# Kernel optimization log

Hardware: AMD Instinct MI355X
Metric: run time of the kernel (lower is better)

The kernel has to match this reference:

```python
import jax, jax.numpy as jnp
import numpy as np

B, NNODES = 65536, 32
D_IN, D_G, D_C, H, D_OUT = 16, 8, 16, 64, 4


def setup_inputs() -> dict:
    key = jax.random.key(0)
    ks = jax.random.split(key, 24)
    N = B * NNODES
    x = jax.random.normal(ks[0], (N, D_IN), jnp.float32)
    other_obs = jax.random.normal(ks[1], (B, D_C), jnp.float32)
    # star graph per batch element with reverse edges: (0->j) and (j->0)
    bs = np.concatenate([np.zeros(NNODES - 1, np.int32), np.arange(1, NNODES, dtype=np.int32)])
    bd = np.concatenate([np.arange(1, NNODES, dtype=np.int32), np.zeros(NNODES - 1, np.int32)])
    offs = (np.arange(B, dtype=np.int32) * NNODES)[:, None]
    src = jnp.asarray((bs[None, :] + offs).reshape(-1))
    dst = jnp.asarray((bd[None, :] + offs).reshape(-1))
    node_seg = jnp.asarray(np.repeat(np.arange(B, dtype=np.int32), NNODES))
    s = 0.1
    p = lambda k, sh: jax.random.normal(k, sh, jnp.float32) * s
    return dict(
        x=x, other_obs=other_obs, src=src, dst=dst, node_seg=node_seg,
        Wp1=p(ks[2], (D_IN, D_G)), bp1=jnp.zeros((D_G,), jnp.float32),
        Ws1=p(ks[3], (D_IN, D_G)), Wn1=p(ks[4], (D_G, D_G)), bc1=jnp.zeros((D_G,), jnp.float32),
        Wp2=p(ks[5], (D_G, D_G)), bp2=jnp.zeros((D_G,), jnp.float32),
        Ws2=p(ks[6], (D_G, D_G)), Wn2=p(ks[7], (D_G, D_G)), bc2=jnp.zeros((D_G,), jnp.float32),
        W1=p(ks[8], (D_C + D_G, H)), bf1=jnp.zeros((H,), jnp.float32),
        W2=p(ks[9], (H, H)), bf2=jnp.zeros((H,), jnp.float32),
        W3=p(ks[10], (H, H)), bf3=jnp.zeros((H,), jnp.float32),
        W4=jax.random.uniform(ks[11], (H, D_OUT), jnp.float32, -0.003, 0.003),
        bf4=jnp.zeros((D_OUT,), jnp.float32),
    )


def _sage_pool(h, src, dst, Wp, bp, Ws, Wn, bc, num_nodes):
    # DGL SAGEConv aggregator_type='pool': relu(fc_pool(h_src)), scatter-max to dst
    m = jax.nn.relu(h @ Wp + bp)[src]              # [E, D_G]
    agg = jax.ops.segment_max(m, dst, num_segments=num_nodes)
    agg = jnp.where(jnp.isfinite(agg), agg, 0.0)   # empty-neighbor nodes -> 0 (DGL default)
    return h @ Ws + agg @ Wn + bc


def reference(x, other_obs, src, dst, node_seg,
              Wp1, bp1, Ws1, Wn1, bc1,
              Wp2, bp2, Ws2, Wn2, bc2,
              W1, bf1, W2, bf2, W3, bf3, W4, bf4):
    N = x.shape[0]
    Bn = other_obs.shape[0]
    n_per = N // Bn
    h = jnp.tanh(_sage_pool(x, src, dst, Wp1, bp1, Ws1, Wn1, bc1, N))  # conv1 activation=tanh
    h = _sage_pool(h, src, dst, Wp2, bp2, Ws2, Wn2, bc2, N)            # conv2, no activation
    pooled = jax.ops.segment_sum(h, node_seg, num_segments=Bn) / n_per  # AvgPooling (fixed n)
    res = jnp.concatenate([pooled, other_obs], axis=1)
    h1 = jax.nn.relu(res @ W1 + bf1)
    h2 = jax.nn.relu(h1 @ W2 + bf2)
    h3 = jax.nn.relu(h2 @ W3 + bf3)
    return jnp.tanh(h3 @ W4 + bf4)
```

## Files before the change

### kernel.cpp

```cpp
#include <hip/hip_runtime.h>


typedef float v2f __attribute__((ext_vector_type(2)));
__device__ __forceinline__ v2f fma2(v2f a, v2f b, v2f c) {
  return __builtin_elementwise_fma(a, b, c);
}
__device__ __forceinline__ v2f ld2(const float* p) { return *(const v2f*)p; }

__device__ __forceinline__ float fast_tanh(float v) {
  v = fminf(fmaxf(v, -10.f), 10.f);
  float e = exp2f(v * 2.8853900817779268f);
  return 1.f - 2.f * __builtin_amdgcn_rcpf(e + 1.f);
}

template<int CTRL, int RMASK>
__device__ __forceinline__ float dpp0(float v) {
  return __int_as_float(__builtin_amdgcn_update_dpp(
      0, __float_as_int(v), CTRL, RMASK, 0xf, true));
}
__device__ __forceinline__ float red_max32(float t) {
  t = fmaxf(t, dpp0<0x111, 0xf>(t));
  t = fmaxf(t, dpp0<0x112, 0xf>(t));
  t = fmaxf(t, dpp0<0x114, 0xf>(t));
  t = fmaxf(t, dpp0<0x118, 0xf>(t));
  t = fmaxf(t, dpp0<0x142, 0xa>(t));
  return t;
}
__device__ __forceinline__ float red_sum32(float t) {
  t += dpp0<0x111, 0xf>(t);
  t += dpp0<0x112, 0xf>(t);
  t += dpp0<0x114, 0xf>(t);
  t += dpp0<0x118, 0xf>(t);
  t += dpp0<0x142, 0xa>(t);
  return t;
}
__device__ __forceinline__ float bcast31(float v) {
  return __int_as_float(__builtin_amdgcn_ds_swizzle(__float_as_int(v), 0x03E0));
}

__global__ __launch_bounds__(256, 4) void conv_kernel(
    const float* __restrict__ x,
    const float* __restrict__ Wp1, const float* __restrict__ bp1,
    const float* __restrict__ Ws1, const float* __restrict__ Wn1,
    const float* __restrict__ bc1,
    const float* __restrict__ Wp2, const float* __restrict__ bp2,
    float* __restrict__ res) {
  const int lane = threadIdx.x & 63;
  const int pair = blockIdx.x * 4 + (threadIdx.x >> 6);
  const int nl = lane & 31, s = lane >> 5;
  const int node = 31 - nl;
  const int b = pair * 2 + s;
  const bool isn0 = (nl == 31);

  const float4* xp = (const float4*)(x + ((size_t)b * 32 + node) * 16);
  float4 a0 = xp[0], a1 = xp[1], a2 = xp[2], a3 = xp[3];
  float xr[16] = {a0.x,a0.y,a0.z,a0.w, a1.x,a1.y,a1.z,a1.w,
                  a2.x,a2.y,a2.z,a2.w, a3.x,a3.y,a3.z,a3.w};

  v2f mv[4], sv[4];
  #pragma unroll
  for (int i = 0; i < 4; i++) { mv[i] = ld2(bp1 + 2*i); sv[i] = ld2(bc1 + 2*i); }
  #pragma unroll
  for (int f = 0; f < 16; f++) {
    v2f xv = {xr[f], xr[f]};
    #pragma unroll
    for (int i = 0; i < 4; i++) {
      mv[i] = fma2(xv, ld2(Wp1 + f*8 + 2*i), mv[i]);
      sv[i] = fma2(xv, ld2(Ws1 + f*8 + 2*i), sv[i]);
    }
  }
  float m[8];
  #pragma unroll
  for (int i = 0; i < 4; i++) {
    m[2*i]   = fmaxf(mv[i].x, 0.f);
    m[2*i+1] = fmaxf(mv[i].y, 0.f);
  }

  float agg[8];
  #pragma unroll
  for (int g = 0; g < 8; g++) {
    float t = isn0 ? 0.f : m[g];
    t = red_max32(t);
    float b0v = bcast31(m[g]);
    agg[g] = isn0 ? t : b0v;
  }
  #pragma unroll
  for (int j = 0; j < 8; j++) {
    v2f av = {agg[j], agg[j]};
    #pragma unroll
    for (int i = 0; i < 4; i++) sv[i] = fma2(av, ld2(Wn1 + j*8 + 2*i), sv[i]);
  }
  float h[8];
  #pragma unroll
  for (int i = 0; i < 4; i++) {
    h[2*i]   = fast_tanh(sv[i].x);
    h[2*i+1] = fast_tanh(sv[i].y);
  }

  v2f m2v[4];
  #pragma unroll
  for (int i = 0; i < 4; i++) m2v[i] = ld2(bp2 + 2*i);
  #pragma unroll
  for (int j = 0; j < 8; j++) {
    v2f hv = {h[j], h[j]};
    #pragma unroll
    for (int i = 0; i < 4; i++) m2v[i] = fma2(hv, ld2(Wp2 + j*8 + 2*i), m2v[i]);
  }
  float m2[8];
  #pragma unroll
  for (int i = 0; i < 4; i++) {
    m2[2*i]   = fmaxf(m2v[i].x, 0.f);
    m2[2*i+1] = fmaxf(m2v[i].y, 0.f);
  }

  float outv[16];
  #pragma unroll
  for (int g = 0; g < 8; g++) outv[g] = red_sum32(h[g]);
  #pragma unroll
  for (int g = 0; g < 8; g++) {
    float t = isn0 ? 0.f : m2[g];
    t = red_max32(t);
    outv[8+g] = fmaf(31.f, m2[g], t);
  }
  if (isn0) {
    float4* rp = (float4*)(res + (size_t)b * 16);
    rp[0] = make_float4(outv[0],  outv[1],  outv[2],  outv[3]);
    rp[1] = make_float4(outv[4],  outv[5],  outv[6],  outv[7]);
    rp[2] = make_float4(outv[8],  outv[9],  outv[10], outv[11]);
    rp[3] = make_float4(outv[12], outv[13], outv[14], outv[15]);
  }
}

#define HSTR 65
__global__ __launch_bounds__(256, 3) void mlp_kernel(
    const float* __restrict__ res, const float* __restrict__ obs,
    const float* __restrict__ Ws2, const float* __restrict__ Wn2,
    const float* __restrict__ bc2,
    const float* __restrict__ W1, const float* __restrict__ bf1,
    const float* __restrict__ W2, const float* __restrict__ bf2,
    const float* __restrict__ W3, const float* __restrict__ bf3,
    const float* __restrict__ W4, const float* __restrict__ bf4,
    float* __restrict__ out) {
  __shared__ float hx[64 * HSTR];
  const int tid  = threadIdx.x;
  const int lane = tid & 63;
  const int p    = __builtin_amdgcn_readfirstlane(tid >> 6);
  const int b    = blockIdx.x * 64 + lane;
  const int ob0  = p * 16;

  const float4* rp = (const float4*)(res + (size_t)b * 16);
  float4 r0 = rp[0], r1 = rp[1], r2 = rp[2], r3 = rp[3];
  const float4* op = (const float4*)(obs + (size_t)b * 16);
  float4 o0 = op[0], o1 = op[1], o2 = op[2], o3 = op[3];
  float rm[8] = {r0.x,r0.y,r0.z,r0.w, r1.x,r1.y,r1.z,r1.w};
  float ag[8] = {r2.x,r2.y,r2.z,r2.w, r3.x,r3.y,r3.z,r3.w};
  float ob[16] = {o0.x,o0.y,o0.z,o0.w, o1.x,o1.y,o1.z,o1.w,
                  o2.x,o2.y,o2.z,o2.w, o3.x,o3.y,o3.z,o3.w};

  v2f pv[4];
  #pragma unroll
  for (int i = 0; i < 4; i++) pv[i] = (v2f){0.f, 0.f};
  #pragma unroll
  for (int j = 0; j < 8; j++) {
    v2f rv = {rm[j], rm[j]}, av = {ag[j], ag[j]};
    #pragma unroll
    for (int i = 0; i < 4; i++) {
      pv[i] = fma2(rv, ld2(Ws2 + j*8 + 2*i), pv[i]);
      pv[i] = fma2(av, ld2(Wn2 + j*8 + 2*i), pv[i]);
    }
  }
  float pooled[8];
  #pragma unroll
  for (int i = 0; i < 4; i++) {
    pooled[2*i]   = fmaf(pv[i].x, 1.f/32.f, bc2[2*i]);
    pooled[2*i+1] = fmaf(pv[i].y, 1.f/32.f, bc2[2*i+1]);
  }

  v2f acc[8];
  #pragma unroll
  for (int i = 0; i < 8; i++) acc[i] = ld2(bf1 + ob0 + 2*i);
  #pragma unroll
  for (int j = 0; j < 8; j++) {
    v2f sj = {pooled[j], pooled[j]};
    #pragma unroll
    for (int i = 0; i < 8; i++) acc[i] = fma2(sj, ld2(W1 + j*64 + ob0 + 2*i), acc[i]);
  }
  #pragma unroll
  for (int j = 0; j < 16; j++) {
    v2f sj = {ob[j], ob[j]};
    #pragma unroll
    for (int i = 0; i < 8; i++) acc[i] = fma2(sj, ld2(W1 + (8+j)*64 + ob0 + 2*i), acc[i]);
  }
  #pragma unroll
  for (int i = 0; i < 8; i++) {
    hx[lane*HSTR + ob0 + 2*i]   = fmaxf(acc[i].x, 0.f);
    hx[lane*HSTR + ob0 + 2*i+1] = fmaxf(acc[i].y, 0.f);
  }
  __syncthreads();
  float h[64];
  #pragma unroll
  for (int k = 0; k < 64; k++) h[k] = hx[lane*HSTR + k];
  __syncthreads();

  #pragma unroll
  for (int i = 0; i < 8; i++) acc[i] = ld2(bf2 + ob0 + 2*i);
  #pragma unroll
  for (int k = 0; k < 64; k++) {
    v2f hk = {h[k], h[k]};
    #pragma unroll
    for (int i = 0; i < 8; i++) acc[i] = fma2(hk, ld2(W2 + k*64 + ob0 + 2*i), acc[i]);
  }
  #pragma unroll
  for (int i = 0; i < 8; i++) {
    hx[lane*HSTR + ob0 + 2*i]   = fmaxf(acc[i].x, 0.f);
    hx[lane*HSTR + ob0 + 2*i+1] = fmaxf(acc[i].y, 0.f);
  }
  __syncthreads();
  #pragma unroll
  for (int k = 0; k < 64; k++) h[k] = hx[lane*HSTR + k];
  __syncthreads();

  #pragma unroll
  for (int i = 0; i < 8; i++) acc[i] = ld2(bf3 + ob0 + 2*i);
  #pragma unroll
  for (int k = 0; k < 64; k++) {
    v2f hk = {h[k], h[k]};
    #pragma unroll
    for (int i = 0; i < 8; i++) acc[i] = fma2(hk, ld2(W3 + k*64 + ob0 + 2*i), acc[i]);
  }
  #pragma unroll
  for (int i = 0; i < 8; i++) {
    hx[lane*HSTR + ob0 + 2*i]   = fmaxf(acc[i].x, 0.f);
    hx[lane*HSTR + ob0 + 2*i+1] = fmaxf(acc[i].y, 0.f);
  }
  __syncthreads();

  if (p == 0) {
    #pragma unroll
    for (int k = 0; k < 64; k++) h[k] = hx[lane*HSTR + k];
    v2f o4a = ld2(bf4), o4b = ld2(bf4 + 2);
    #pragma unroll
    for (int k = 0; k < 64; k++) {
      v2f hk = {h[k], h[k]};
      o4a = fma2(hk, ld2(W4 + k*4),     o4a);
      o4b = fma2(hk, ld2(W4 + k*4 + 2), o4b);
    }
    ((float4*)out)[b] = make_float4(fast_tanh(o4a.x), fast_tanh(o4a.y),
                                    fast_tanh(o4b.x), fast_tanh(o4b.y));
  }
}

extern "C" void kernel_launch(void* const* d_in, const int* in_sizes, int n_in,
                              void* d_out, int out_size, void* d_ws, size_t ws_size,
                              hipStream_t stream) {
  const float* x   = (const float*)d_in[0];
  const float* obs = (const float*)d_in[1];
  const float* Wp1 = (const float*)d_in[5];
  const float* bp1 = (const float*)d_in[6];
  const float* Ws1 = (const float*)d_in[7];
  const float* Wn1 = (const float*)d_in[8];
  const float* bc1 = (const float*)d_in[9];
  const float* Wp2 = (const float*)d_in[10];
  const float* bp2 = (const float*)d_in[11];
  const float* Ws2 = (const float*)d_in[12];
  const float* Wn2 = (const float*)d_in[13];
  const float* bc2 = (const float*)d_in[14];
  const float* W1  = (const float*)d_in[15];
  const float* bf1 = (const float*)d_in[16];
  const float* W2  = (const float*)d_in[17];
  const float* bf2 = (const float*)d_in[18];
  const float* W3  = (const float*)d_in[19];
  const float* bf3 = (const float*)d_in[20];
  const float* W4  = (const float*)d_in[21];
  const float* bf4 = (const float*)d_in[22];
  float* res = (float*)d_ws;
  float* out = (float*)d_out;

  hipLaunchKernelGGL(conv_kernel, dim3(8192), dim3(256), 0, stream,
                     x, Wp1, bp1, Ws1, Wn1, bc1, Wp2, bp2, res);
  hipLaunchKernelGGL(mlp_kernel, dim3(1024), dim3(256), 0, stream,
                     res, obs, Ws2, Wn2, bc2, W1, bf1, W2, bf2, W3, bf3, W4, bf4, out);
}
```

Baseline: 280.0 us.

## Fuse conv and MLP kernels into one kernel with shared-memory handoff

Merges the graph-conv kernel and the MLP kernel into a single launch. Each 256-thread block now loops over 8 batch pairs per wave, prefetching the next x tile while it computes the current one, and stages the per-graph results in shared memory instead of a global workspace. This removes one launch and the global write and read of the intermediate. In exchange the grid drops to 1024 blocks with serialized conv work per wave, the launch bound rises from 3 to 4 blocks per CU for the MLP part, and register and LDS pressure both increase.

After: 299.6 us. 1.07x slower.

```diff
diff --git a/kernel.cpp b/kernel.cpp
--- a/kernel.cpp
+++ b/kernel.cpp
@@ -38,122 +38,130 @@
   return __int_as_float(__builtin_amdgcn_ds_swizzle(__float_as_int(v), 0x03E0));
 }
 
-__global__ __launch_bounds__(256, 4) void conv_kernel(
-    const float* __restrict__ x,
+#define RSTR 17
+#define HSTR 65
+
+__global__ __launch_bounds__(256, 4) void fused_gnn(
+    const float* __restrict__ x,   const float* __restrict__ obs,
     const float* __restrict__ Wp1, const float* __restrict__ bp1,
     const float* __restrict__ Ws1, const float* __restrict__ Wn1,
     const float* __restrict__ bc1,
     const float* __restrict__ Wp2, const float* __restrict__ bp2,
-    float* __restrict__ res) {
-  const int lane = threadIdx.x & 63;
-  const int pair = blockIdx.x * 4 + (threadIdx.x >> 6);
-  const int nl = lane & 31, s = lane >> 5;
-  const int node = 31 - nl;
-  const int b = pair * 2 + s;
-  const bool isn0 = (nl == 31);
-
-  const float4* xp = (const float4*)(x + ((size_t)b * 32 + node) * 16);
-  float4 a0 = xp[0], a1 = xp[1], a2 = xp[2], a3 = xp[3];
-  float xr[16] = {a0.x,a0.y,a0.z,a0.w, a1.x,a1.y,a1.z,a1.w,
-                  a2.x,a2.y,a2.z,a2.w, a3.x,a3.y,a3.z,a3.w};
-
-  v2f mv[4], sv[4];
-  #pragma unroll
-  for (int i = 0; i < 4; i++) { mv[i] = ld2(bp1 + 2*i); sv[i] = ld2(bc1 + 2*i); }
-  #pragma unroll
-  for (int f = 0; f < 16; f++) {
-    v2f xv = {xr[f], xr[f]};
-    #pragma unroll
-    for (int i = 0; i < 4; i++) {
-      mv[i] = fma2(xv, ld2(Wp1 + f*8 + 2*i), mv[i]);
-      sv[i] = fma2(xv, ld2(Ws1 + f*8 + 2*i), sv[i]);
-    }
-  }
-  float m[8];
-  #pragma unroll
-  for (int i = 0; i < 4; i++) {
-    m[2*i]   = fmaxf(mv[i].x, 0.f);
-    m[2*i+1] = fmaxf(mv[i].y, 0.f);
-  }
-
-  float agg[8];
-  #pragma unroll
-  for (int g = 0; g < 8; g++) {
-    float t = isn0 ? 0.f : m[g];
-    t = red_max32(t);
-    float b0v = bcast31(m[g]);
-    agg[g] = isn0 ? t : b0v;
-  }
-  #pragma unroll
-  for (int j = 0; j < 8; j++) {
-    v2f av = {agg[j], agg[j]};
-    #pragma unroll
-    for (int i = 0; i < 4; i++) sv[i] = fma2(av, ld2(Wn1 + j*8 + 2*i), sv[i]);
-  }
-  float h[8];
-  #pragma unroll
-  for (int i = 0; i < 4; i++) {
-    h[2*i]   = fast_tanh(sv[i].x);
-    h[2*i+1] = fast_tanh(sv[i].y);
-  }
-
-  v2f m2v[4];
-  #pragma unroll
-  for (int i = 0; i < 4; i++) m2v[i] = ld2(bp2 + 2*i);
-  #pragma unroll
-  for (int j = 0; j < 8; j++) {
-    v2f hv = {h[j], h[j]};
-    #pragma unroll
-    for (int i = 0; i < 4; i++) m2v[i] = fma2(hv, ld2(Wp2 + j*8 + 2*i), m2v[i]);
-  }
-  float m2[8];
-  #pragma unroll
-  for (int i = 0; i < 4; i++) {
-    m2[2*i]   = fmaxf(m2v[i].x, 0.f);
-    m2[2*i+1] = fmaxf(m2v[i].y, 0.f);
-  }
-
-  float outv[16];
-  #pragma unroll
-  for (int g = 0; g < 8; g++) outv[g] = red_sum32(h[g]);
-  #pragma unroll
-  for (int g = 0; g < 8; g++) {
-    float t = isn0 ? 0.f : m2[g];
-    t = red_max32(t);
-    outv[8+g] = fmaf(31.f, m2[g], t);
-  }
-  if (isn0) {
-    float4* rp = (float4*)(res + (size_t)b * 16);
-    rp[0] = make_float4(outv[0],  outv[1],  outv[2],  outv[3]);
-    rp[1] = make_float4(outv[4],  outv[5],  outv[6],  outv[7]);
-    rp[2] = make_float4(outv[8],  outv[9],  outv[10], outv[11]);
-    rp[3] = make_float4(outv[12], outv[13], outv[14], outv[15]);
-  }
-}
-
-#define HSTR 65
-__global__ __launch_bounds__(256, 3) void mlp_kernel(
-    const float* __restrict__ res, const float* __restrict__ obs,
     const float* __restrict__ Ws2, const float* __restrict__ Wn2,
     const float* __restrict__ bc2,
-    const float* __restrict__ W1, const float* __restrict__ bf1,
-    const float* __restrict__ W2, const float* __restrict__ bf2,
-    const float* __restrict__ W3, const float* __restrict__ bf3,
-    const float* __restrict__ W4, const float* __restrict__ bf4,
+    const float* __restrict__ W1,  const float* __restrict__ bf1,
+    const float* __restrict__ W2,  const float* __restrict__ bf2,
+    const float* __restrict__ W3,  const float* __restrict__ bf3,
+    const float* __restrict__ W4,  const float* __restrict__ bf4,
     float* __restrict__ out) {
+  __shared__ float resT[64 * RSTR];
   __shared__ float hx[64 * HSTR];
+
   const int tid  = threadIdx.x;
   const int lane = tid & 63;
   const int p    = __builtin_amdgcn_readfirstlane(tid >> 6);
-  const int b    = blockIdx.x * 64 + lane;
-  const int ob0  = p * 16;
-
-  const float4* rp = (const float4*)(res + (size_t)b * 16);
-  float4 r0 = rp[0], r1 = rp[1], r2 = rp[2], r3 = rp[3];
-  const float4* op = (const float4*)(obs + (size_t)b * 16);
+  const int nl   = lane & 31, s = lane >> 5;
+  const int node = 31 - nl;
+  const bool isn0 = (nl == 31);
+  const int b0   = blockIdx.x * 64;
+
+  const float4* op = (const float4*)(obs + (size_t)(b0 + lane) * 16);
   float4 o0 = op[0], o1 = op[1], o2 = op[2], o3 = op[3];
-  float rm[8] = {r0.x,r0.y,r0.z,r0.w, r1.x,r1.y,r1.z,r1.w};
-  float ag[8] = {r2.x,r2.y,r2.z,r2.w, r3.x,r3.y,r3.z,r3.w};
+
+  const float* xb = x + (((size_t)(b0 + p * 16 + s)) * 32 + node) * 16;
+  float4 c0, c1, c2, c3;
+  { const float4* xp = (const float4*)xb; c0 = xp[0]; c1 = xp[1]; c2 = xp[2]; c3 = xp[3]; }
+
+  for (int j = 0; j < 8; ++j) {
+    float4 nx0, nx1, nx2, nx3;
+    if (j < 7) {
+      const float4* xp = (const float4*)(xb + (size_t)(j + 1) * 1024);
+      nx0 = xp[0]; nx1 = xp[1]; nx2 = xp[2]; nx3 = xp[3];
+    }
+    float xr[16] = {c0.x,c0.y,c0.z,c0.w, c1.x,c1.y,c1.z,c1.w,
+                    c2.x,c2.y,c2.z,c2.w, c3.x,c3.y,c3.z,c3.w};
+
+    v2f mv[4], sv[4];
+    #pragma unroll
+    for (int i = 0; i < 4; i++) { mv[i] = ld2(bp1 + 2*i); sv[i] = ld2(bc1 + 2*i); }
+    #pragma unroll
+    for (int f = 0; f < 16; f++) {
+      v2f xv = {xr[f], xr[f]};
+      #pragma unroll
+      for (int i = 0; i < 4; i++) {
+        mv[i] = fma2(xv, ld2(Wp1 + f*8 + 2*i), mv[i]);
+        sv[i] = fma2(xv, ld2(Ws1 + f*8 + 2*i), sv[i]);
+      }
+    }
+    float m[8];
+    #pragma unroll
+    for (int i = 0; i < 4; i++) {
+      m[2*i]   = fmaxf(mv[i].x, 0.f);
+      m[2*i+1] = fmaxf(mv[i].y, 0.f);
+    }
+
+    float agg[8];
+    #pragma unroll
+    for (int g = 0; g < 8; g++) {
+      float t = isn0 ? 0.f : m[g];
+      t = red_max32(t);
+      float b0v = bcast31(m[g]);
+      agg[g] = isn0 ? t : b0v;
+    }
+    #pragma unroll
+    for (int jj = 0; jj < 8; jj++) {
+      v2f av = {agg[jj], agg[jj]};
+      #pragma unroll
+      for (int i = 0; i < 4; i++) sv[i] = fma2(av, ld2(Wn1 + jj*8 + 2*i), sv[i]);
+    }
+    float h[8];
+    #pragma unroll
+    for (int i = 0; i < 4; i++) {
+      h[2*i]   = fast_tanh(sv[i].x);
+      h[2*i+1] = fast_tanh(sv[i].y);
+    }
+
+    v2f m2v[4];
+    #pragma unroll
+    for (int i = 0; i < 4; i++) m2v[i] = ld2(bp2 + 2*i);
+    #pragma unroll
+    for (int jj = 0; jj < 8; jj++) {
+      v2f hv = {h[jj], h[jj]};
+      #pragma unroll
+      for (int i = 0; i < 4; i++) m2v[i] = fma2(hv, ld2(Wp2 + jj*8 + 2*i), m2v[i]);
+    }
+    float m2[8];
+    #pragma unroll
+    for (int i = 0; i < 4; i++) {
+      m2[2*i]   = fmaxf(m2v[i].x, 0.f);
+      m2[2*i+1] = fmaxf(m2v[i].y, 0.f);
+    }
+
+    float outv[16];
+    #pragma unroll
+    for (int g = 0; g < 8; g++) outv[g] = red_sum32(h[g]);
+    #pragma unroll
+    for (int g = 0; g < 8; g++) {
+      float t = isn0 ? 0.f : m2[g];
+      t = red_max32(t);
+      outv[8+g] = fmaf(31.f, m2[g], t);
+    }
+    if (isn0) {
+      const int bib = (p * 8 + j) * 2 + s;
+      #pragma unroll
+      for (int i = 0; i < 16; i++) resT[bib * RSTR + i] = outv[i];
+    }
+    if (j < 7) { c0 = nx0; c1 = nx1; c2 = nx2; c3 = nx3; }
+  }
+  __syncthreads();
+
+  const int ob0 = p * 16;
+  float rm[8], ag[8];
+  #pragma unroll
+  for (int jj = 0; jj < 8; jj++) {
+    rm[jj] = resT[lane * RSTR + jj];
+    ag[jj] = resT[lane * RSTR + 8 + jj];
+  }
   float ob[16] = {o0.x,o0.y,o0.z,o0.w, o1.x,o1.y,o1.z,o1.w,
                   o2.x,o2.y,o2.z,o2.w, o3.x,o3.y,o3.z,o3.w};
 
@@ -161,12 +169,12 @@
   #pragma unroll
   for (int i = 0; i < 4; i++) pv[i] = (v2f){0.f, 0.f};
   #pragma unroll
-  for (int j = 0; j < 8; j++) {
-    v2f rv = {rm[j], rm[j]}, av = {ag[j], ag[j]};
-    #pragma unroll
-    for (int i = 0; i < 4; i++) {
-      pv[i] = fma2(rv, ld2(Ws2 + j*8 + 2*i), pv[i]);
-      pv[i] = fma2(av, ld2(Wn2 + j*8 + 2*i), pv[i]);
+  for (int jj = 0; jj < 8; jj++) {
+    v2f rv = {rm[jj], rm[jj]}, av = {ag[jj], ag[jj]};
+    #pragma unroll
+    for (int i = 0; i < 4; i++) {
+      pv[i] = fma2(rv, ld2(Ws2 + jj*8 + 2*i), pv[i]);
+      pv[i] = fma2(av, ld2(Wn2 + jj*8 + 2*i), pv[i]);
     }
   }
   float pooled[8];
@@ -180,16 +188,16 @@
   #pragma unroll
   for (int i = 0; i < 8; i++) acc[i] = ld2(bf1 + ob0 + 2*i);
   #pragma unroll
-  for (int j = 0; j < 8; j++) {
-    v2f sj = {pooled[j], pooled[j]};
-    #pragma unroll
-    for (int i = 0; i < 8; i++) acc[i] = fma2(sj, ld2(W1 + j*64 + ob0 + 2*i), acc[i]);
-  }
-  #pragma unroll
-  for (int j = 0; j < 16; j++) {
-    v2f sj = {ob[j], ob[j]};
-    #pragma unroll
-    for (int i = 0; i < 8; i++) acc[i] = fma2(sj, ld2(W1 + (8+j)*64 + ob0 + 2*i), acc[i]);
+  for (int jj = 0; jj < 8; jj++) {
+    v2f sj = {pooled[jj], pooled[jj]};
+    #pragma unroll
+    for (int i = 0; i < 8; i++) acc[i] = fma2(sj, ld2(W1 + jj*64 + ob0 + 2*i), acc[i]);
+  }
+  #pragma unroll
+  for (int jj = 0; jj < 16; jj++) {
+    v2f sj = {ob[jj], ob[jj]};
+    #pragma unroll
+    for (int i = 0; i < 8; i++) acc[i] = fma2(sj, ld2(W1 + (8+jj)*64 + ob0 + 2*i), acc[i]);
   }
   #pragma unroll
   for (int i = 0; i < 8; i++) {
@@ -245,8 +253,8 @@
       o4a = fma2(hk, ld2(W4 + k*4),     o4a);
       o4b = fma2(hk, ld2(W4 + k*4 + 2), o4b);
     }
-    ((float4*)out)[b] = make_float4(fast_tanh(o4a.x), fast_tanh(o4a.y),
-                                    fast_tanh(o4b.x), fast_tanh(o4b.y));
+    ((float4*)out)[b0 + lane] = make_float4(fast_tanh(o4a.x), fast_tanh(o4a.y),
+                                            fast_tanh(o4b.x), fast_tanh(o4b.y));
   }
 }
 
@@ -273,11 +281,9 @@
   const float* bf3 = (const float*)d_in[20];
   const float* W4  = (const float*)d_in[21];
   const float* bf4 = (const float*)d_in[22];
-  float* res = (float*)d_ws;
   float* out = (float*)d_out;
 
-  hipLaunchKernelGGL(conv_kernel, dim3(8192), dim3(256), 0, stream,
-                     x, Wp1, bp1, Ws1, Wn1, bc1, Wp2, bp2, res);
-  hipLaunchKernelGGL(mlp_kernel, dim3(1024), dim3(256), 0, stream,
-                     res, obs, Ws2, Wn2, bc2, W1, bf1, W2, bf2, W3, bf3, W4, bf4, out);
-}
+  hipLaunchKernelGGL(fused_gnn, dim3(1024), dim3(256), 0, stream,
+                     x, obs, Wp1, bp1, Ws1, Wn1, bc1, Wp2, bp2, Ws2, Wn2, bc2,
+                     W1, bf1, W2, bf2, W3, bf3, W4, bf4, out);
+}
```

## Process two graph pairs per wave in conv and split MLP across eight waves

Applied to the files above, without the earlier changes.

The conv kernel now has each wave handle two pairs of batch elements. All x loads for both are issued up front so memory latency overlaps across the unrolled iterations, and the grid is halved. The MLP kernel moves to 512-thread blocks where each wave computes 8 output columns instead of 16, which cuts per-thread accumulator registers and adds more waves per block. The tanh input clamp is also removed; it relied on rcp handling large exponents, and the unclamped exp2 can overflow to inf for large inputs.

After: 293.8 us. 4.9% more time.

```diff
diff --git a/kernel.cpp b/kernel.cpp
--- a/kernel.cpp
+++ b/kernel.cpp
@@ -8,7 +8,6 @@
 __device__ __forceinline__ v2f ld2(const float* p) { return *(const v2f*)p; }
 
 __device__ __forceinline__ float fast_tanh(float v) {
-  v = fminf(fmaxf(v, -10.f), 10.f);
   float e = exp2f(v * 2.8853900817779268f);
   return 1.f - 2.f * __builtin_amdgcn_rcpf(e + 1.f);
 }
@@ -46,93 +45,105 @@
     const float* __restrict__ Wp2, const float* __restrict__ bp2,
     float* __restrict__ res) {
   const int lane = threadIdx.x & 63;
-  const int pair = blockIdx.x * 4 + (threadIdx.x >> 6);
+  const int wid  = blockIdx.x * 4 + (threadIdx.x >> 6);
   const int nl = lane & 31, s = lane >> 5;
   const int node = 31 - nl;
-  const int b = pair * 2 + s;
   const bool isn0 = (nl == 31);
 
-  const float4* xp = (const float4*)(x + ((size_t)b * 32 + node) * 16);
-  float4 a0 = xp[0], a1 = xp[1], a2 = xp[2], a3 = xp[3];
-  float xr[16] = {a0.x,a0.y,a0.z,a0.w, a1.x,a1.y,a1.z,a1.w,
-                  a2.x,a2.y,a2.z,a2.w, a3.x,a3.y,a3.z,a3.w};
-
-  v2f mv[4], sv[4];
-  #pragma unroll
-  for (int i = 0; i < 4; i++) { mv[i] = ld2(bp1 + 2*i); sv[i] = ld2(bc1 + 2*i); }
-  #pragma unroll
-  for (int f = 0; f < 16; f++) {
-    v2f xv = {xr[f], xr[f]};
-    #pragma unroll
-    for (int i = 0; i < 4; i++) {
-      mv[i] = fma2(xv, ld2(Wp1 + f*8 + 2*i), mv[i]);
-      sv[i] = fma2(xv, ld2(Ws1 + f*8 + 2*i), sv[i]);
-    }
-  }
-  float m[8];
-  #pragma unroll
-  for (int i = 0; i < 4; i++) {
-    m[2*i]   = fmaxf(mv[i].x, 0.f);
-    m[2*i+1] = fmaxf(mv[i].y, 0.f);
-  }
-
-  float agg[8];
-  #pragma unroll
-  for (int g = 0; g < 8; g++) {
-    float t = isn0 ? 0.f : m[g];
-    t = red_max32(t);
-    float b0v = bcast31(m[g]);
-    agg[g] = isn0 ? t : b0v;
-  }
-  #pragma unroll
-  for (int j = 0; j < 8; j++) {
-    v2f av = {agg[j], agg[j]};
-    #pragma unroll
-    for (int i = 0; i < 4; i++) sv[i] = fma2(av, ld2(Wn1 + j*8 + 2*i), sv[i]);
-  }
-  float h[8];
-  #pragma unroll
-  for (int i = 0; i < 4; i++) {
-    h[2*i]   = fast_tanh(sv[i].x);
-    h[2*i+1] = fast_tanh(sv[i].y);
-  }
-
-  v2f m2v[4];
-  #pragma unroll
-  for (int i = 0; i < 4; i++) m2v[i] = ld2(bp2 + 2*i);
-  #pragma unroll
-  for (int j = 0; j < 8; j++) {
-    v2f hv = {h[j], h[j]};
-    #pragma unroll
-    for (int i = 0; i < 4; i++) m2v[i] = fma2(hv, ld2(Wp2 + j*8 + 2*i), m2v[i]);
-  }
-  float m2[8];
-  #pragma unroll
-  for (int i = 0; i < 4; i++) {
-    m2[2*i]   = fmaxf(m2v[i].x, 0.f);
-    m2[2*i+1] = fmaxf(m2v[i].y, 0.f);
-  }
-
-  float outv[16];
-  #pragma unroll
-  for (int g = 0; g < 8; g++) outv[g] = red_sum32(h[g]);
-  #pragma unroll
-  for (int g = 0; g < 8; g++) {
-    float t = isn0 ? 0.f : m2[g];
-    t = red_max32(t);
-    outv[8+g] = fmaf(31.f, m2[g], t);
-  }
-  if (isn0) {
-    float4* rp = (float4*)(res + (size_t)b * 16);
-    rp[0] = make_float4(outv[0],  outv[1],  outv[2],  outv[3]);
-    rp[1] = make_float4(outv[4],  outv[5],  outv[6],  outv[7]);
-    rp[2] = make_float4(outv[8],  outv[9],  outv[10], outv[11]);
-    rp[3] = make_float4(outv[12], outv[13], outv[14], outv[15]);
+  const int bA = wid * 4 + s;
+  const float* xbA = x + (((size_t)bA) * 32 + node) * 16;
+  const float* xbB = xbA + 2 * 32 * 16;
+
+  const float4* xpA = (const float4*)xbA;
+  const float4* xpB = (const float4*)xbB;
+  float4 A0 = xpA[0], A1 = xpA[1], A2 = xpA[2], A3 = xpA[3];
+  float4 B0 = xpB[0], B1 = xpB[1], B2 = xpB[2], B3 = xpB[3];
+
+  #pragma unroll
+  for (int pp = 0; pp < 2; ++pp) {
+    const int b = (pp == 0) ? bA : bA + 2;
+    float4 c0 = (pp == 0) ? A0 : B0, c1 = (pp == 0) ? A1 : B1;
+    float4 c2 = (pp == 0) ? A2 : B2, c3 = (pp == 0) ? A3 : B3;
+    float xr[16] = {c0.x,c0.y,c0.z,c0.w, c1.x,c1.y,c1.z,c1.w,
+                    c2.x,c2.y,c2.z,c2.w, c3.x,c3.y,c3.z,c3.w};
+
+    v2f mv[4], sv[4];
+    #pragma unroll
+    for (int i = 0; i < 4; i++) { mv[i] = ld2(bp1 + 2*i); sv[i] = ld2(bc1 + 2*i); }
+    #pragma unroll
+    for (int f = 0; f < 16; f++) {
+      v2f xv = {xr[f], xr[f]};
+      #pragma unroll
+      for (int i = 0; i < 4; i++) {
+        mv[i] = fma2(xv, ld2(Wp1 + f*8 + 2*i), mv[i]);
+        sv[i] = fma2(xv, ld2(Ws1 + f*8 + 2*i), sv[i]);
+      }
+    }
+    float m[8];
+    #pragma unroll
+    for (int i = 0; i < 4; i++) {
+      m[2*i]   = fmaxf(mv[i].x, 0.f);
+      m[2*i+1] = fmaxf(mv[i].y, 0.f);
+    }
+
+    float agg[8];
+    #pragma unroll
+    for (int g = 0; g < 8; g++) {
+      float t = isn0 ? 0.f : m[g];
+      t = red_max32(t);
+      float b0v = bcast31(m[g]);
+      agg[g] = isn0 ? t : b0v;
+    }
+    #pragma unroll
+    for (int jj = 0; jj < 8; jj++) {
+      v2f av = {agg[jj], agg[jj]};
+      #pragma unroll
+      for (int i = 0; i < 4; i++) sv[i] = fma2(av, ld2(Wn1 + jj*8 + 2*i), sv[i]);
+    }
+    float h[8];
+    #pragma unroll
+    for (int i = 0; i < 4; i++) {
+      h[2*i]   = fast_tanh(sv[i].x);
+      h[2*i+1] = fast_tanh(sv[i].y);
+    }
+
+    v2f m2v[4];
+    #pragma unroll
+    for (int i = 0; i < 4; i++) m2v[i] = ld2(bp2 + 2*i);
+    #pragma unroll
+    for (int jj = 0; jj < 8; jj++) {
+      v2f hv = {h[jj], h[jj]};
+      #pragma unroll
+      for (int i = 0; i < 4; i++) m2v[i] = fma2(hv, ld2(Wp2 + jj*8 + 2*i), m2v[i]);
+    }
+    float m2[8];
+    #pragma unroll
+    for (int i = 0; i < 4; i++) {
+      m2[2*i]   = fmaxf(m2v[i].x, 0.f);
+      m2[2*i+1] = fmaxf(m2v[i].y, 0.f);
+    }
+
+    float outv[16];
+    #pragma unroll
+    for (int g = 0; g < 8; g++) outv[g] = red_sum32(h[g]);
+    #pragma unroll
+    for (int g = 0; g < 8; g++) {
+      float t = isn0 ? 0.f : m2[g];
+      t = red_max32(t);
+      outv[8+g] = fmaf(31.f, m2[g], t);
+    }
+    if (isn0) {
+      float4* rp = (float4*)(res + (size_t)b * 16);
+      rp[0] = make_float4(outv[0],  outv[1],  outv[2],  outv[3]);
+      rp[1] = make_float4(outv[4],  outv[5],  outv[6],  outv[7]);
+      rp[2] = make_float4(outv[8],  outv[9],  outv[10], outv[11]);
+      rp[3] = make_float4(outv[12], outv[13], outv[14], outv[15]);
+    }
   }
 }
 
 #define HSTR 65
-__global__ __launch_bounds__(256, 3) void mlp_kernel(
+__global__ __launch_bounds__(512, 2) void mlp_kernel(
     const float* __restrict__ res, const float* __restrict__ obs,
     const float* __restrict__ Ws2, const float* __restrict__ Wn2,
     const float* __restrict__ bc2,
@@ -146,7 +157,7 @@
   const int lane = tid & 63;
   const int p    = __builtin_amdgcn_readfirstlane(tid >> 6);
   const int b    = blockIdx.x * 64 + lane;
-  const int ob0  = p * 16;
+  const int ob0  = p * 8;
 
   const float4* rp = (const float4*)(res + (size_t)b * 16);
   float4 r0 = rp[0], r1 = rp[1], r2 = rp[2], r3 = rp[3];
@@ -161,12 +172,12 @@
   #pragma unroll
   for (int i = 0; i < 4; i++) pv[i] = (v2f){0.f, 0.f};
   #pragma unroll
-  for (int j = 0; j < 8; j++) {
-    v2f rv = {rm[j], rm[j]}, av = {ag[j], ag[j]};
-    #pragma unroll
-    for (int i = 0; i < 4; i++) {
-      pv[i] = fma2(rv, ld2(Ws2 + j*8 + 2*i), pv[i]);
-      pv[i] = fma2(av, ld2(Wn2 + j*8 + 2*i), pv[i]);
+  for (int jj = 0; jj < 8; jj++) {
+    v2f rv = {rm[jj], rm[jj]}, av = {ag[jj], ag[jj]};
+    #pragma unroll
+    for (int i = 0; i < 4; i++) {
+      pv[i] = fma2(rv, ld2(Ws2 + jj*8 + 2*i), pv[i]);
+      pv[i] = fma2(av, ld2(Wn2 + jj*8 + 2*i), pv[i]);
     }
   }
   float pooled[8];
@@ -176,23 +187,23 @@
     pooled[2*i+1] = fmaf(pv[i].y, 1.f/32.f, bc2[2*i+1]);
   }
 
-  v2f acc[8];
-  #pragma unroll
-  for (int i = 0; i < 8; i++) acc[i] = ld2(bf1 + ob0 + 2*i);
-  #pragma unroll
-  for (int j = 0; j < 8; j++) {
-    v2f sj = {pooled[j], pooled[j]};
-    #pragma unroll
-    for (int i = 0; i < 8; i++) acc[i] = fma2(sj, ld2(W1 + j*64 + ob0 + 2*i), acc[i]);
-  }
-  #pragma unroll
-  for (int j = 0; j < 16; j++) {
-    v2f sj = {ob[j], ob[j]};
-    #pragma unroll
-    for (int i = 0; i < 8; i++) acc[i] = fma2(sj, ld2(W1 + (8+j)*64 + ob0 + 2*i), acc[i]);
-  }
-  #pragma unroll
-  for (int i = 0; i < 8; i++) {
+  v2f acc[4];
+  #pragma unroll
+  for (int i = 0; i < 4; i++) acc[i] = ld2(bf1 + ob0 + 2*i);
+  #pragma unroll
+  for (int jj = 0; jj < 8; jj++) {
+    v2f sj = {pooled[jj], pooled[jj]};
+    #pragma unroll
+    for (int i = 0; i < 4; i++) acc[i] = fma2(sj, ld2(W1 + jj*64 + ob0 + 2*i), acc[i]);
+  }
+  #pragma unroll
+  for (int jj = 0; jj < 16; jj++) {
+    v2f sj = {ob[jj], ob[jj]};
+    #pragma unroll
+    for (int i = 0; i < 4; i++) acc[i] = fma2(sj, ld2(W1 + (8+jj)*64 + ob0 + 2*i), acc[i]);
+  }
+  #pragma unroll
+  for (int i = 0; i < 4; i++) {
     hx[lane*HSTR + ob0 + 2*i]   = fmaxf(acc[i].x, 0.f);
     hx[lane*HSTR + ob0 + 2*i+1] = fmaxf(acc[i].y, 0.f);
   }
@@ -203,15 +214,15 @@
   __syncthreads();
 
   #pragma unroll
-  for (int i = 0; i < 8; i++) acc[i] = ld2(bf2 + ob0 + 2*i);
+  for (int i = 0; i < 4; i++) acc[i] = ld2(bf2 + ob0 + 2*i);
   #pragma unroll
   for (int k = 0; k < 64; k++) {
     v2f hk = {h[k], h[k]};
     #pragma unroll
-    for (int i = 0; i < 8; i++) acc[i] = fma2(hk, ld2(W2 + k*64 + ob0 + 2*i), acc[i]);
-  }
-  #pragma unroll
-  for (int i = 0; i < 8; i++) {
+    for (int i = 0; i < 4; i++) acc[i] = fma2(hk, ld2(W2 + k*64 + ob0 + 2*i), acc[i]);
+  }
+  #pragma unroll
+  for (int i = 0; i < 4; i++) {
     hx[lane*HSTR + ob0 + 2*i]   = fmaxf(acc[i].x, 0.f);
     hx[lane*HSTR + ob0 + 2*i+1] = fmaxf(acc[i].y, 0.f);
   }
@@ -221,15 +232,15 @@
   __syncthreads();
 
   #pragma unroll
-  for (int i = 0; i < 8; i++) acc[i] = ld2(bf3 + ob0 + 2*i);
+  for (int i = 0; i < 4; i++) acc[i] = ld2(bf3 + ob0 + 2*i);
   #pragma unroll
   for (int k = 0; k < 64; k++) {
     v2f hk = {h[k], h[k]};
     #pragma unroll
-    for (int i = 0; i < 8; i++) acc[i] = fma2(hk, ld2(W3 + k*64 + ob0 + 2*i), acc[i]);
-  }
-  #pragma unroll
-  for (int i = 0; i < 8; i++) {
+    for (int i = 0; i < 4; i++) acc[i] = fma2(hk, ld2(W3 + k*64 + ob0 + 2*i), acc[i]);
+  }
+  #pragma unroll
+  for (int i = 0; i < 4; i++) {
     hx[lane*HSTR + ob0 + 2*i]   = fmaxf(acc[i].x, 0.f);
     hx[lane*HSTR + ob0 + 2*i+1] = fmaxf(acc[i].y, 0.f);
   }
@@ -276,8 +287,8 @@
   float* res = (float*)d_ws;
   float* out = (float*)d_out;
 
-  hipLaunchKernelGGL(conv_kernel, dim3(8192), dim3(256), 0, stream,
+  hipLaunchKernelGGL(conv_kernel, dim3(4096), dim3(256), 0, stream,
                      x, Wp1, bp1, Ws1, Wn1, bc1, Wp2, bp2, res);
-  hipLaunchKernelGGL(mlp_kernel, dim3(1024), dim3(256), 0, stream,
+  hipLaunchKernelGGL(mlp_kernel, dim3(1024), dim3(512), 0, stream,
                      res, obs, Ws2, Wn2, bc2, W1, bf1, W2, bf2, W3, bf3, W4, bf4, out);
 }
```

## Process two batch rows per thread in MLP kernel to reuse weight loads

Applied to the files above, without the earlier changes.

The MLP kernel now handles 128 batch rows per block, so each thread computes two rows and every weight load feeds two sets of accumulators. The first stage (pooled plus obs) is computed by half the threads and staged in shared memory, and activations are read from LDS inside the loops instead of being copied into a register array. The grid is halved to match. The tanh input clamp is also dropped to save instructions, which relies on exp2f overflow still giving the right saturated values, and shared memory and register use go up, which may lower occupancy.

Measured after the change: 282.1 us. No clear change (+0.7%).

```diff
diff --git a/kernel.cpp b/kernel.cpp
--- a/kernel.cpp
+++ b/kernel.cpp
@@ -8,7 +8,6 @@
 __device__ __forceinline__ v2f ld2(const float* p) { return *(const v2f*)p; }
 
 __device__ __forceinline__ float fast_tanh(float v) {
-  v = fminf(fmaxf(v, -10.f), 10.f);
   float e = exp2f(v * 2.8853900817779268f);
   return 1.f - 2.f * __builtin_amdgcn_rcpf(e + 1.f);
 }
@@ -49,8 +48,8 @@
   const int pair = blockIdx.x * 4 + (threadIdx.x >> 6);
   const int nl = lane & 31, s = lane >> 5;
   const int node = 31 - nl;
+  const bool isn0 = (nl == 31);
   const int b = pair * 2 + s;
-  const bool isn0 = (nl == 31);
 
   const float4* xp = (const float4*)(x + ((size_t)b * 32 + node) * 16);
   float4 a0 = xp[0], a1 = xp[1], a2 = xp[2], a3 = xp[3];
@@ -85,10 +84,10 @@
     agg[g] = isn0 ? t : b0v;
   }
   #pragma unroll
-  for (int j = 0; j < 8; j++) {
-    v2f av = {agg[j], agg[j]};
-    #pragma unroll
-    for (int i = 0; i < 4; i++) sv[i] = fma2(av, ld2(Wn1 + j*8 + 2*i), sv[i]);
+  for (int jj = 0; jj < 8; jj++) {
+    v2f av = {agg[jj], agg[jj]};
+    #pragma unroll
+    for (int i = 0; i < 4; i++) sv[i] = fma2(av, ld2(Wn1 + jj*8 + 2*i), sv[i]);
   }
   float h[8];
   #pragma unroll
@@ -101,10 +100,10 @@
   #pragma unroll
   for (int i = 0; i < 4; i++) m2v[i] = ld2(bp2 + 2*i);
   #pragma unroll
-  for (int j = 0; j < 8; j++) {
-    v2f hv = {h[j], h[j]};
-    #pragma unroll
-    for (int i = 0; i < 4; i++) m2v[i] = fma2(hv, ld2(Wp2 + j*8 + 2*i), m2v[i]);
+  for (int jj = 0; jj < 8; jj++) {
+    v2f hv = {h[jj], h[jj]};
+    #pragma unroll
+    for (int i = 0; i < 4; i++) m2v[i] = fma2(hv, ld2(Wp2 + jj*8 + 2*i), m2v[i]);
   }
   float m2[8];
   #pragma unroll
@@ -131,7 +130,8 @@
   }
 }
 
-#define HSTR 65
+#define H0S 25
+#define HXS 65
 __global__ __launch_bounds__(256, 3) void mlp_kernel(
     const float* __restrict__ res, const float* __restrict__ obs,
     const float* __restrict__ Ws2, const float* __restrict__ Wn2,
@@ -141,112 +141,133 @@
     const float* __restrict__ W3, const float* __restrict__ bf3,
     const float* __restrict__ W4, const float* __restrict__ bf4,
     float* __restrict__ out) {
-  __shared__ float hx[64 * HSTR];
+  __shared__ float h0[128 * H0S];
+  __shared__ float hx[128 * HXS];
   const int tid  = threadIdx.x;
   const int lane = tid & 63;
   const int p    = __builtin_amdgcn_readfirstlane(tid >> 6);
-  const int b    = blockIdx.x * 64 + lane;
   const int ob0  = p * 16;
-
-  const float4* rp = (const float4*)(res + (size_t)b * 16);
-  float4 r0 = rp[0], r1 = rp[1], r2 = rp[2], r3 = rp[3];
-  const float4* op = (const float4*)(obs + (size_t)b * 16);
-  float4 o0 = op[0], o1 = op[1], o2 = op[2], o3 = op[3];
-  float rm[8] = {r0.x,r0.y,r0.z,r0.w, r1.x,r1.y,r1.z,r1.w};
-  float ag[8] = {r2.x,r2.y,r2.z,r2.w, r3.x,r3.y,r3.z,r3.w};
-  float ob[16] = {o0.x,o0.y,o0.z,o0.w, o1.x,o1.y,o1.z,o1.w,
-                  o2.x,o2.y,o2.z,o2.w, o3.x,o3.y,o3.z,o3.w};
-
-  v2f pv[4];
-  #pragma unroll
-  for (int i = 0; i < 4; i++) pv[i] = (v2f){0.f, 0.f};
-  #pragma unroll
-  for (int j = 0; j < 8; j++) {
-    v2f rv = {rm[j], rm[j]}, av = {ag[j], ag[j]};
+  const int bbase = blockIdx.x * 128;
+
+  if (tid < 128) {
+    const float4* rp = (const float4*)(res + (size_t)(bbase + tid) * 16);
+    float4 r0 = rp[0], r1 = rp[1], r2 = rp[2], r3 = rp[3];
+    const float4* op = (const float4*)(obs + (size_t)(bbase + tid) * 16);
+    float4 o0 = op[0], o1 = op[1], o2 = op[2], o3 = op[3];
+    float rm[8] = {r0.x,r0.y,r0.z,r0.w, r1.x,r1.y,r1.z,r1.w};
+    float ag[8] = {r2.x,r2.y,r2.z,r2.w, r3.x,r3.y,r3.z,r3.w};
+    v2f pv[4];
+    #pragma unroll
+    for (int i = 0; i < 4; i++) pv[i] = (v2f){0.f, 0.f};
+    #pragma unroll
+    for (int j = 0; j < 8; j++) {
+      v2f rv = {rm[j], rm[j]}, av = {ag[j], ag[j]};
+      #pragma unroll
+      for (int i = 0; i < 4; i++) {
+        pv[i] = fma2(rv, ld2(Ws2 + j*8 + 2*i), pv[i]);
+        pv[i] = fma2(av, ld2(Wn2 + j*8 + 2*i), pv[i]);
+      }
+    }
+    float* hr = h0 + tid * H0S;
     #pragma unroll
     for (int i = 0; i < 4; i++) {
-      pv[i] = fma2(rv, ld2(Ws2 + j*8 + 2*i), pv[i]);
-      pv[i] = fma2(av, ld2(Wn2 + j*8 + 2*i), pv[i]);
-    }
-  }
-  float pooled[8];
-  #pragma unroll
-  for (int i = 0; i < 4; i++) {
-    pooled[2*i]   = fmaf(pv[i].x, 1.f/32.f, bc2[2*i]);
-    pooled[2*i+1] = fmaf(pv[i].y, 1.f/32.f, bc2[2*i+1]);
-  }
-
-  v2f acc[8];
-  #pragma unroll
-  for (int i = 0; i < 8; i++) acc[i] = ld2(bf1 + ob0 + 2*i);
-  #pragma unroll
-  for (int j = 0; j < 8; j++) {
-    v2f sj = {pooled[j], pooled[j]};
-    #pragma unroll
-    for (int i = 0; i < 8; i++) acc[i] = fma2(sj, ld2(W1 + j*64 + ob0 + 2*i), acc[i]);
-  }
-  #pragma unroll
-  for (int j = 0; j < 16; j++) {
-    v2f sj = {ob[j], ob[j]};
-    #pragma unroll
-    for (int i = 0; i < 8; i++) acc[i] = fma2(sj, ld2(W1 + (8+j)*64 + ob0 + 2*i), acc[i]);
+      hr[2*i]   = fmaf(pv[i].x, 1.f/32.f, bc2[2*i]);
+      hr[2*i+1] = fmaf(pv[i].y, 1.f/32.f, bc2[2*i+1]);
+    }
+    hr[8]=o0.x;  hr[9]=o0.y;  hr[10]=o0.z; hr[11]=o0.w;
+    hr[12]=o1.x; hr[13]=o1.y; hr[14]=o1.z; hr[15]=o1.w;
+    hr[16]=o2.x; hr[17]=o2.y; hr[18]=o2.z; hr[19]=o2.w;
+    hr[20]=o3.x; hr[21]=o3.y; hr[22]=o3.z; hr[23]=o3.w;
+  }
+  __syncthreads();
+
+  const float* h0a = h0 + lane * H0S;
+  const float* h0b = h0 + (64 + lane) * H0S;
+  float* hxa = hx + lane * HXS;
+  float* hxb = hx + (64 + lane) * HXS;
+
+  v2f acc0[8], acc1[8];
+  #pragma unroll
+  for (int i = 0; i < 8; i++) { acc0[i] = ld2(bf1 + ob0 + 2*i); acc1[i] = acc0[i]; }
+  #pragma unroll
+  for (int k = 0; k < 24; k++) {
+    v2f a0 = {h0a[k], h0a[k]}, a1 = {h0b[k], h0b[k]};
+    #pragma unroll
+    for (int i = 0; i < 8; i++) {
+      v2f w = ld2(W1 + k*64 + ob0 + 2*i);
+      acc0[i] = fma2(a0, w, acc0[i]);
+      acc1[i] = fma2(a1, w, acc1[i]);
+    }
   }
   #pragma unroll
   for (int i = 0; i < 8; i++) {
-    hx[lane*HSTR + ob0 + 2*i]   = fmaxf(acc[i].x, 0.f);
-    hx[lane*HSTR + ob0 + 2*i+1] = fmaxf(acc[i].y, 0.f);
-  }
-  __syncthreads();
-  float h[64];
-  #pragma unroll
-  for (int k = 0; k < 64; k++) h[k] = hx[lane*HSTR + k];
-  __syncthreads();
-
-  #pragma unroll
-  for (int i = 0; i < 8; i++) acc[i] = ld2(bf2 + ob0 + 2*i);
+    hxa[ob0 + 2*i]   = fmaxf(acc0[i].x, 0.f);
+    hxa[ob0 + 2*i+1] = fmaxf(acc0[i].y, 0.f);
+    hxb[ob0 + 2*i]   = fmaxf(acc1[i].x, 0.f);
+    hxb[ob0 + 2*i+1] = fmaxf(acc1[i].y, 0.f);
+  }
+  __syncthreads();
+
+  #pragma unroll
+  for (int i = 0; i < 8; i++) { acc0[i] = ld2(bf2 + ob0 + 2*i); acc1[i] = acc0[i]; }
   #pragma unroll
   for (int k = 0; k < 64; k++) {
-    v2f hk = {h[k], h[k]};
-    #pragma unroll
-    for (int i = 0; i < 8; i++) acc[i] = fma2(hk, ld2(W2 + k*64 + ob0 + 2*i), acc[i]);
-  }
+    v2f a0 = {hxa[k], hxa[k]}, a1 = {hxb[k], hxb[k]};
+    #pragma unroll
+    for (int i = 0; i < 8; i++) {
+      v2f w = ld2(W2 + k*64 + ob0 + 2*i);
+      acc0[i] = fma2(a0, w, acc0[i]);
+      acc1[i] = fma2(a1, w, acc1[i]);
+    }
+  }
+  __syncthreads();
   #pragma unroll
   for (int i = 0; i < 8; i++) {
-    hx[lane*HSTR + ob0 + 2*i]   = fmaxf(acc[i].x, 0.f);
-    hx[lane*HSTR + ob0 + 2*i+1] = fmaxf(acc[i].y, 0.f);
-  }
-  __syncthreads();
-  #pragma unroll
-  for (int k = 0; k < 64; k++) h[k] = hx[lane*HSTR + k];
-  __syncthreads();
-
-  #pragma unroll
-  for (int i = 0; i < 8; i++) acc[i] = ld2(bf3 + ob0 + 2*i);
+    hxa[ob0 + 2*i]   = fmaxf(acc0[i].x, 0.f);
+    hxa[ob0 + 2*i+1] = fmaxf(acc0[i].y, 0.f);
+    hxb[ob0 + 2*i]   = fmaxf(acc1[i].x, 0.f);
+    hxb[ob0 + 2*i+1] = fmaxf(acc1[i].y, 0.f);
+  }
+  __syncthreads();
+
+  #pragma unroll
+  for (int i = 0; i < 8; i++) { acc0[i] = ld2(bf3 + ob0 + 2*i); acc1[i] = acc0[i]; }
   #pragma unroll
   for (int k = 0; k < 64; k++) {
-    v2f hk = {h[k], h[k]};
-    #pragma unroll
-    for (int i = 0; i < 8; i++) acc[i] = fma2(hk, ld2(W3 + k*64 + ob0 + 2*i), acc[i]);
-  }
+    v2f a0 = {hxa[k], hxa[k]}, a1 = {hxb[k], hxb[k]};
+    #pragma unroll
+    for (int i = 0; i < 8; i++) {
+      v2f w = ld2(W3 + k*64 + ob0 + 2*i);
+      acc0[i] = fma2(a0, w, acc0[i]);
+      acc1[i] = fma2(a1, w, acc1[i]);
+    }
+  }
+  __syncthreads();
   #pragma unroll
   for (int i = 0; i < 8; i++) {
-    hx[lane*HSTR + ob0 + 2*i]   = fmaxf(acc[i].x, 0.f);
-    hx[lane*HSTR + ob0 + 2*i+1] = fmaxf(acc[i].y, 0.f);
+    hxa[ob0 + 2*i]   = fmaxf(acc0[i].x, 0.f);
+    hxa[ob0 + 2*i+1] = fmaxf(acc0[i].y, 0.f);
+    hxb[ob0 + 2*i]   = fmaxf(acc1[i].x, 0.f);
+    hxb[ob0 + 2*i+1] = fmaxf(acc1[i].y, 0.f);
   }
   __syncthreads();
 
   if (p == 0) {
-    #pragma unroll
-    for (int k = 0; k < 64; k++) h[k] = hx[lane*HSTR + k];
-    v2f o4a = ld2(bf4), o4b = ld2(bf4 + 2);
+    v2f qa0 = ld2(bf4), qb0 = ld2(bf4 + 2);
+    v2f qa1 = qa0, qb1 = qb0;
     #pragma unroll
     for (int k = 0; k < 64; k++) {
-      v2f hk = {h[k], h[k]};
-      o4a = fma2(hk, ld2(W4 + k*4),     o4a);
-      o4b = fma2(hk, ld2(W4 + k*4 + 2), o4b);
-    }
-    ((float4*)out)[b] = make_float4(fast_tanh(o4a.x), fast_tanh(o4a.y),
-                                    fast_tanh(o4b.x), fast_tanh(o4b.y));
+      v2f a0 = {hxa[k], hxa[k]}, a1 = {hxb[k], hxb[k]};
+      v2f w0 = ld2(W4 + k*4), w1 = ld2(W4 + k*4 + 2);
+      qa0 = fma2(a0, w0, qa0); qb0 = fma2(a0, w1, qb0);
+      qa1 = fma2(a1, w0, qa1); qb1 = fma2(a1, w1, qb1);
+    }
+    ((float4*)out)[bbase + lane] =
+        make_float4(fast_tanh(qa0.x), fast_tanh(qa0.y),
+                    fast_tanh(qb0.x), fast_tanh(qb0.y));
+    ((float4*)out)[bbase + 64 + lane] =
+        make_float4(fast_tanh(qa1.x), fast_tanh(qa1.y),
+                    fast_tanh(qb1.x), fast_tanh(qb1.y));
   }
 }
 
@@ -278,6 +299,6 @@
 
   hipLaunchKernelGGL(conv_kernel, dim3(8192), dim3(256), 0, stream,
                      x, Wp1, bp1, Ws1, Wn1, bc1, Wp2, bp2, res);
-  hipLaunchKernelGGL(mlp_kernel, dim3(1024), dim3(256), 0, stream,
+  hipLaunchKernelGGL(mlp_kernel, dim3(512), dim3(256), 0, stream,
                      res, obs, Ws2, Wn2, bc2, W1, bf1, W2, bf2, W3, bf3, W4, bf4, out);
 }
```
